# Kernel tuning notes

Hardware: AMD Instinct MI355X
Metric: run time of the kernel (lower is better)

Reference implementation:

```python
import jax, jax.numpy as jnp
import numpy as np

N_NODES = 100000
N_EDGES = 1600000
D = 64  # input_dim = hidden_dim = output_dim
EPS = 1e-12


def _sage_layer(x, src, dst, wl, bl, wr, br):
    # gather messages from source nodes: [E, D]
    msg = x[src]
    # scatter-mean onto destination nodes
    s = jax.ops.segment_sum(msg, dst, num_segments=x.shape[0])
    cnt = jax.ops.segment_sum(jnp.ones((src.shape[0], 1), x.dtype), dst, num_segments=x.shape[0])
    prop = s / jnp.maximum(cnt, 1.0)
    out = x @ wl.T + bl + prop @ wr.T + br
    # F.normalize(out, p=2, dim=1)
    norm = jnp.sqrt(jnp.sum(out * out, axis=1, keepdims=True))
    return out / jnp.maximum(norm, EPS)


def setup_inputs() -> dict:
    key = jax.random.key(0)
    ks = jax.random.split(key, 12)
    d = D

    def lin(k, fan_in, fan_out):
        bound = 1.0 / np.sqrt(fan_in)
        kw, kb = jax.random.split(k)
        w = jax.random.uniform(kw, (fan_out, fan_in), jnp.float32, -bound, bound)
        b = jax.random.uniform(kb, (fan_out,), jnp.float32, -bound, bound)
        return w, b

    x = jax.random.normal(ks[0], (N_NODES, d), jnp.float32)
    edge_index = jax.random.randint(ks[1], (2, N_EDGES), 0, N_NODES, jnp.int64)

    w1l, b1l = lin(ks[2], d, d)
    w1r, b1r = lin(ks[3], d, d)
    w2l, b2l = lin(ks[4], d, d)
    w2r, b2r = lin(ks[5], d, d)
    wp1, bp1 = lin(ks[6], d, d)
    wp2, bp2 = lin(ks[7], d, d)

    return {"x": x, "edge_index": edge_index,
            "w1l": w1l, "b1l": b1l, "w1r": w1r, "b1r": b1r,
            "w2l": w2l, "b2l": b2l, "w2r": w2r, "b2r": b2r,
            "wp1": wp1, "bp1": bp1, "wp2": wp2, "bp2": bp2}


def reference(x, edge_index, w1l, b1l, w1r, b1r, w2l, b2l, w2r, b2r, wp1, bp1, wp2, bp2):
    src = edge_index[0]
    dst = edge_index[1]
    # layer 1: GraphSage -> relu (dropout is identity in eval)
    h = _sage_layer(x, src, dst, w1l, b1l, w1r, b1r)
    h = jax.nn.relu(h)
    # layer 2
    h = _sage_layer(h, src, dst, w2l, b2l, w2r, b2r)
    h = jax.nn.relu(h)
    # post_mp: Linear -> Dropout(identity) -> Linear; emb=True so no log_softmax
    h = h @ wp1.T + bp1
    h = h @ wp2.T + bp2
    return h
```

## Files before the change

### kernel.cpp

```cpp
#include <hip/hip_runtime.h>

#define NN 100000
#define NE 1600000
#define DD 64
#define NB 196
#define BKT 512
#define CAP 9000
#define NOCT 12500
#define NH 391
#define NG1 1024

__global__ void init_kernel(int* __restrict__ gcursor) {
  int t = threadIdx.x;
  if (t < NB) gcursor[t] = t * CAP;
}

__launch_bounds__(256)
__global__ void scatter2_kernel(const int* __restrict__ src, const int* __restrict__ dst,
                                int* __restrict__ gcursor, int2* __restrict__ pairs) {
  __shared__ int lh[NB];
  __shared__ int lbase[NB];
  __shared__ int lcur[NB];
  const int NQ = NE / 4;
  int t = blockIdx.x * 256 + threadIdx.x;
  const int nt = NH * 256;
  for (int i = threadIdx.x; i < NB; i += 256) lh[i] = 0;
  __syncthreads();
  int4 dv[4], sv[4];
  bool pv[4];
  #pragma unroll
  for (int k = 0; k < 4; ++k) {
    int idx = t + k * nt;
    pv[k] = idx < NQ;
    if (pv[k]) {
      dv[k] = reinterpret_cast<const int4*>(dst)[idx];
      sv[k] = reinterpret_cast<const int4*>(src)[idx];
      atomicAdd(&lh[dv[k].x >> 9], 1);
      atomicAdd(&lh[dv[k].y >> 9], 1);
      atomicAdd(&lh[dv[k].z >> 9], 1);
      atomicAdd(&lh[dv[k].w >> 9], 1);
    }
  }
  __syncthreads();
  for (int i = threadIdx.x; i < NB; i += 256) {
    lcur[i] = 0;
    lbase[i] = lh[i] ? atomicAdd(&gcursor[i], lh[i]) : 0;
  }
  __syncthreads();
  #pragma unroll
  for (int k = 0; k < 4; ++k) {
    if (pv[k]) {
      int b;
      b = dv[k].x >> 9; pairs[lbase[b] + atomicAdd(&lcur[b], 1)] = make_int2(sv[k].x, dv[k].x);
      b = dv[k].y >> 9; pairs[lbase[b] + atomicAdd(&lcur[b], 1)] = make_int2(sv[k].y, dv[k].y);
      b = dv[k].z >> 9; pairs[lbase[b] + atomicAdd(&lcur[b], 1)] = make_int2(sv[k].z, dv[k].z);
      b = dv[k].w >> 9; pairs[lbase[b] + atomicAdd(&lcur[b], 1)] = make_int2(sv[k].w, dv[k].w);
    }
  }
}

__launch_bounds__(256)
__global__ void csr_kernel(const int2* __restrict__ pairs, const int* __restrict__ gcursor,
                           int* __restrict__ deg, int* __restrict__ off,
                           int* __restrict__ adj) {
  __shared__ int lh[BKT];
  __shared__ int wsum[4];
  int b = blockIdx.x;
  int t = threadIdx.x;
  int rs = b * CAP, re = gcursor[b];
  lh[2 * t] = 0;
  lh[2 * t + 1] = 0;
  __syncthreads();
  for (int i = rs + t; i < re; i += 256)
    atomicAdd(&lh[pairs[i].y - b * BKT], 1);
  __syncthreads();
  int lane = t & 63, w = t >> 6;
  int h0 = lh[2 * t], h1 = lh[2 * t + 1];
  int s = h0 + h1, incl = s;
  #pragma unroll
  for (int o = 1; o < 64; o <<= 1) {
    int u = __shfl_up(incl, o, 64);
    if (lane >= o) incl += u;
  }
  if (lane == 63) wsum[w] = incl;
  __syncthreads();
  int prefix = 0;
  for (int u = 0; u < w; ++u) prefix += wsum[u];
  int excl = prefix + incl - s;
  int n0 = b * BKT + 2 * t, n1 = n0 + 1;
  if (n0 < NN) { deg[n0] = h0; off[n0] = rs + excl; }
  if (n1 < NN) { deg[n1] = h1; off[n1] = rs + excl + h0; }
  lh[2 * t] = excl;
  lh[2 * t + 1] = excl + h0;
  __syncthreads();
  for (int i = rs + t; i < re; i += 256) {
    int2 e = pairs[i];
    int pos = atomicAdd(&lh[e.y - b * BKT], 1);
    adj[rs + pos] = e.x;
  }
}

__launch_bounds__(256)
__global__ void selfgemm_kernel(const float* __restrict__ x,
                                const float* __restrict__ wl,
                                const float* __restrict__ bl,
                                const float* __restrict__ br,
                                float* __restrict__ tmp,
                                const float* __restrict__ wp1, const float* __restrict__ bp1,
                                const float* __restrict__ wp2, const float* __restrict__ bp2,
                                float* __restrict__ wcT, float* __restrict__ bc) {
  __shared__ float wA[DD * DD] __attribute__((aligned(16)));
  __shared__ float sp[4][8][DD] __attribute__((aligned(16)));
  int bid = blockIdx.x;
  if (bid < NG1) {
    int tid = threadIdx.x;
    int j = tid & 63;
    int w = tid >> 6;
    for (int i = tid; i < DD * DD; i += 256) {
      int jj = i >> 6, kk = i & 63;
      wA[kk * DD + jj] = wl[i];
    }
    float bias = bl[j] + br[j];
    __syncthreads();
    const int ngrp = 3125;
    for (int grp = bid; grp < ngrp; grp += NG1) {
      int n0 = (grp * 4 + w) * 8;
      #pragma unroll
      for (int i = 0; i < 8; ++i) sp[w][i][j] = x[(size_t)(n0 + i) * DD + j];
      float acc[8];
      #pragma unroll
      for (int i = 0; i < 8; ++i) acc[i] = bias;
      #pragma unroll
      for (int q = 0; q < 16; ++q) {
        int kb = q * 4;
        float w0 = wA[(kb + 0) * DD + j];
        float w1v = wA[(kb + 1) * DD + j];
        float w2v = wA[(kb + 2) * DD + j];
        float w3v = wA[(kb + 3) * DD + j];
        #pragma unroll
        for (int i = 0; i < 8; ++i) {
          float4 sv = *(const float4*)&sp[w][i][kb];
          float a = acc[i];
          a = fmaf(sv.x, w0, a);
          a = fmaf(sv.y, w1v, a);
          a = fmaf(sv.z, w2v, a);
          a = fmaf(sv.w, w3v, a);
          acc[i] = a;
        }
      }
      #pragma unroll
      for (int i = 0; i < 8; ++i) tmp[(size_t)(n0 + i) * DD + j] = acc[i];
    }
  } else {
    int t = threadIdx.x;
    for (int idx = t; idx < DD * DD; idx += 256) {
      int jp = idx >> 6, k = idx & 63;
      float s = 0.f;
      #pragma unroll
      for (int m = 0; m < DD; ++m) s = fmaf(wp2[jp * DD + m], wp1[m * DD + k], s);
      wcT[k * DD + jp] = s;
    }
    if (t < DD) {
      float s = bp2[t];
      #pragma unroll
      for (int m = 0; m < DD; ++m) s = fmaf(wp2[t * DD + m], bp1[m], s);
      bc[t] = s;
    }
  }
}

__launch_bounds__(256)
__global__ void gather_kernel(const float* __restrict__ x,
                              const int* __restrict__ off,
                              const int* __restrict__ deg,
                              const int* __restrict__ adj,
                              float* __restrict__ prop) {
  const float4* X = reinterpret_cast<const float4*>(x);
  int wid = (blockIdx.x * 256 + threadIdx.x) >> 6;
  int nwaves = (gridDim.x * 256) >> 6;
  int lane = threadIdx.x & 63;
  int g = lane >> 4;
  int s = lane & 15;
  const int NQUAD = NN / 4;
  for (int q = wid; q < NQUAD; q += nwaves) {
    int n = q * 4 + g;
    int start = off[n];
    int d = deg[n];
    float4 a0 = {0,0,0,0}, a1 = {0,0,0,0}, a2 = {0,0,0,0}, a3 = {0,0,0,0};
    int t = 0;
    for (; t + 4 <= d; t += 4) {
      int i0 = adj[start + t + 0];
      int i1 = adj[start + t + 1];
      int i2 = adj[start + t + 2];
      int i3 = adj[start + t + 3];
      float4 v0 = X[i0 * 16 + s];
      float4 v1 = X[i1 * 16 + s];
      float4 v2 = X[i2 * 16 + s];
      float4 v3 = X[i3 * 16 + s];
      a0.x += v0.x; a0.y += v0.y; a0.z += v0.z; a0.w += v0.w;
      a1.x += v1.x; a1.y += v1.y; a1.z += v1.z; a1.w += v1.w;
      a2.x += v2.x; a2.y += v2.y; a2.z += v2.z; a2.w += v2.w;
      a3.x += v3.x; a3.y += v3.y; a3.z += v3.z; a3.w += v3.w;
    }
    if (t < d) {
      int dm = d - 1;
      int u1 = (t + 1 < d) ? t + 1 : dm;
      int u2 = (t + 2 < d) ? t + 2 : dm;
      int i0 = adj[start + t];
      int i1 = adj[start + u1];
      int i2 = adj[start + u2];
      float4 v0 = X[i0 * 16 + s];
      float4 v1 = X[i1 * 16 + s];
      float4 v2 = X[i2 * 16 + s];
      a0.x += v0.x; a0.y += v0.y; a0.z += v0.z; a0.w += v0.w;
      if (t + 1 < d) { a1.x += v1.x; a1.y += v1.y; a1.z += v1.z; a1.w += v1.w; }
      if (t + 2 < d) { a2.x += v2.x; a2.y += v2.y; a2.z += v2.z; a2.w += v2.w; }
    }
    float rc = 1.0f / fmaxf((float)d, 1.0f);
    float4 r;
    r.x = ((a0.x + a1.x) + (a2.x + a3.x)) * rc;
    r.y = ((a0.y + a1.y) + (a2.y + a3.y)) * rc;
    r.z = ((a0.z + a1.z) + (a2.z + a3.z)) * rc;
    r.w = ((a0.w + a1.w) + (a2.w + a3.w)) * rc;
    reinterpret_cast<float4*>(prop)[n * 16 + s] = r;
  }
}

__launch_bounds__(512, 4)
__global__ void gemm_light_kernel(float* __restrict__ out,
                                  const float* __restrict__ prop,
                                  const float* __restrict__ wr) {
  __shared__ float wrA[DD * DD] __attribute__((aligned(16)));
  __shared__ float pp[8][8][DD] __attribute__((aligned(16)));
  int tid = threadIdx.x;
  int j = tid & 63;
  int w = tid >> 6;

  for (int i = tid; i < DD * DD; i += 512) {
    int jj = i >> 6, kk = i & 63;
    wrA[kk * DD + jj] = wr[i];
  }
  __syncthreads();

  const int ngrp = (NOCT + 7) / 8;
  for (int grp = blockIdx.x; grp < ngrp; grp += gridDim.x) {
    int o = grp * 8 + w;
    if (o >= NOCT) continue;
    int n0 = o * 8;

    float acc[8];
    #pragma unroll
    for (int i = 0; i < 8; ++i) {
      pp[w][i][j] = prop[(size_t)(n0 + i) * DD + j];
      acc[i] = out[(size_t)(n0 + i) * DD + j];
    }

    #pragma unroll
    for (int q = 0; q < 16; ++q) {
      int kb = q * 4;
      float w0 = wrA[(kb + 0) * DD + j];
      float w1v = wrA[(kb + 1) * DD + j];
      float w2v = wrA[(kb + 2) * DD + j];
      float w3v = wrA[(kb + 3) * DD + j];
      #pragma unroll
      for (int i = 0; i < 8; ++i) {
        float4 pv = *(const float4*)&pp[w][i][kb];
        float a = acc[i];
        a = fmaf(pv.x, w0, a);
        a = fmaf(pv.y, w1v, a);
        a = fmaf(pv.z, w2v, a);
        a = fmaf(pv.w, w3v, a);
        acc[i] = a;
      }
    }

    #pragma unroll
    for (int i = 0; i < 8; ++i) {
      float a = acc[i];
      float ss = a * a;
      #pragma unroll
      for (int o2 = 32; o2 > 0; o2 >>= 1) ss += __shfl_xor(ss, o2, 64);
      float ov = a / fmaxf(sqrtf(ss), 1e-12f);
      ov = fmaxf(ov, 0.0f);
      out[(size_t)(n0 + i) * DD + j] = ov;
    }
  }
}

__launch_bounds__(512, 4)
__global__ void sage_post_kernel(const float* __restrict__ xin,
                                 const float* __restrict__ prop,
                                 const float* __restrict__ wl,
                                 const float* __restrict__ bl,
                                 const float* __restrict__ wr,
                                 const float* __restrict__ br,
                                 const float* __restrict__ wcT,
                                 const float* __restrict__ bc,
                                 float* __restrict__ out) {
  __shared__ float wlA[DD * DD] __attribute__((aligned(16)));
  __shared__ float wrA[DD * DD] __attribute__((aligned(16)));
  __shared__ float sp[8][8][DD] __attribute__((aligned(16)));
  __shared__ float pp[8][8][DD] __attribute__((aligned(16)));
  int tid = threadIdx.x;
  int j = tid & 63;
  int w = tid >> 6;

  for (int i = tid; i < DD * DD; i += 512) {
    int jj = i >> 6, kk = i & 63;
    wlA[kk * DD + jj] = wl[i];
    wrA[kk * DD + jj] = wr[i];
  }
  float bias = bl[j] + br[j];
  float bcv = bc[j];
  __syncthreads();

  const int ngrp = (NOCT + 7) / 8;
  for (int grp = blockIdx.x; grp < ngrp; grp += gridDim.x) {
    int o = grp * 8 + w;
    if (o >= NOCT) continue;
    int n0 = o * 8;

    #pragma unroll
    for (int i = 0; i < 8; ++i) {
      sp[w][i][j] = xin[(size_t)(n0 + i) * DD + j];
      pp[w][i][j] = prop[(size_t)(n0 + i) * DD + j];
    }

    float acc[8];
    #pragma unroll
    for (int i = 0; i < 8; ++i) acc[i] = bias;

    #pragma unroll
    for (int q = 0; q < 16; ++q) {
      int kb = q * 4;
      float wl0 = wlA[(kb + 0) * DD + j];
      float wl1 = wlA[(kb + 1) * DD + j];
      float wl2 = wlA[(kb + 2) * DD + j];
      float wl3 = wlA[(kb + 3) * DD + j];
      float wr0 = wrA[(kb + 0) * DD + j];
      float wr1 = wrA[(kb + 1) * DD + j];
      float wr2 = wrA[(kb + 2) * DD + j];
      float wr3 = wrA[(kb + 3) * DD + j];
      #pragma unroll
      for (int i = 0; i < 8; ++i) {
        float4 sv = *(const float4*)&sp[w][i][kb];
        float4 pv = *(const float4*)&pp[w][i][kb];
        float a = acc[i];
        a = fmaf(sv.x, wl0, a);
        a = fmaf(sv.y, wl1, a);
        a = fmaf(sv.z, wl2, a);
        a = fmaf(sv.w, wl3, a);
        a = fmaf(pv.x, wr0, a);
        a = fmaf(pv.y, wr1, a);
        a = fmaf(pv.z, wr2, a);
        a = fmaf(pv.w, wr3, a);
        acc[i] = a;
      }
    }

    #pragma unroll
    for (int i = 0; i < 8; ++i) {
      float a = acc[i];
      float ss = a * a;
      #pragma unroll
      for (int o2 = 32; o2 > 0; o2 >>= 1) ss += __shfl_xor(ss, o2, 64);
      float ov = a / fmaxf(sqrtf(ss), 1e-12f);
      ov = fmaxf(ov, 0.0f);
      sp[w][i][j] = ov;
    }

    float acc2[8];
    #pragma unroll
    for (int i = 0; i < 8; ++i) acc2[i] = bcv;
    #pragma unroll
    for (int q = 0; q < 16; ++q) {
      int kb = q * 4;
      float w0 = wcT[(kb + 0) * DD + j];
      float w1v = wcT[(kb + 1) * DD + j];
      float w2v = wcT[(kb + 2) * DD + j];
      float w3v = wcT[(kb + 3) * DD + j];
      #pragma unroll
      for (int i = 0; i < 8; ++i) {
        float4 hv = *(const float4*)&sp[w][i][kb];
        float a = acc2[i];
        a = fmaf(hv.x, w0, a);
        a = fmaf(hv.y, w1v, a);
        a = fmaf(hv.z, w2v, a);
        a = fmaf(hv.w, w3v, a);
        acc2[i] = a;
      }
    }
    #pragma unroll
    for (int i = 0; i < 8; ++i) out[(size_t)(n0 + i) * DD + j] = acc2[i];
  }
}

extern "C" void kernel_launch(void* const* d_in, const int* in_sizes, int n_in,
                              void* d_out, int out_size, void* d_ws, size_t ws_size,
                              hipStream_t stream) {
  const float* x   = (const float*)d_in[0];
  const int*   ei  = (const int*)d_in[1];
  const float* w1l = (const float*)d_in[2];
  const float* b1l = (const float*)d_in[3];
  const float* w1r = (const float*)d_in[4];
  const float* b1r = (const float*)d_in[5];
  const float* w2l = (const float*)d_in[6];
  const float* b2l = (const float*)d_in[7];
  const float* w2r = (const float*)d_in[8];
  const float* b2r = (const float*)d_in[9];
  const float* wp1 = (const float*)d_in[10];
  const float* bp1 = (const float*)d_in[11];
  const float* wp2 = (const float*)d_in[12];
  const float* bp2 = (const float*)d_in[13];
  float* out = (float*)d_out;

  const int* src = ei;
  const int* dst = ei + NE;

  int* deg     = (int*)d_ws;
  int* off     = deg + 102400;
  int* aux     = off + 102400;
  int* gcursor = aux;
  float* wcT   = (float*)(aux + 1024);
  float* bc    = wcT + 4096;
  int* adj     = (int*)(bc + 1024);
  float* prop  = (float*)(adj + NB * CAP);
  int2* pairs  = (int2*)prop;

  init_kernel<<<1, 256, 0, stream>>>(gcursor);
  scatter2_kernel<<<NH, 256, 0, stream>>>(src, dst, gcursor, pairs);
  csr_kernel<<<NB, 256, 0, stream>>>(pairs, gcursor, deg, off, adj);

  selfgemm_kernel<<<NG1 + 1, 256, 0, stream>>>(x, w1l, b1l, b1r, out,
                                               wp1, bp1, wp2, bp2, wcT, bc);

  gather_kernel<<<2048, 256, 0, stream>>>(x, off, deg, adj, prop);
  gemm_light_kernel<<<1024, 512, 0, stream>>>(out, prop, w1r);

  gather_kernel<<<2048, 256, 0, stream>>>(out, off, deg, adj, prop);
  sage_post_kernel<<<512, 512, 0, stream>>>(out, prop, w2l, b2l, w2r, b2r,
                                            wcT, bc, out);
}
```

Measured before the change: 299.9 us.

## Read activations directly from global memory and pack weights as float4 in LDS

The three dense GEMM kernels stop staging the activation rows (x, prop) into shared memory. Each thread now reads float4 chunks straight from global memory, as wave-uniform broadcast loads. Weight matrices are stored in an interleaved float4 layout so each k-quad is one 16-byte LDS read, and the combined post-MLP weight is written in the same layout. Launch bounds rise to 6 blocks per unit and sage_post gets more blocks. The aim is to cut LDS traffic and footprint to raise occupancy, at the risk of more global or L1 load instructions and register pressure.

```diff
diff --git a/kernel.cpp b/kernel.cpp
--- a/kernel.cpp
+++ b/kernel.cpp
@@ -100,7 +100,7 @@
   }
 }
 
-__launch_bounds__(256)
+__launch_bounds__(256, 6)
 __global__ void selfgemm_kernel(const float* __restrict__ x,
                                 const float* __restrict__ wl,
                                 const float* __restrict__ bl,
@@ -108,43 +108,38 @@
                                 float* __restrict__ tmp,
                                 const float* __restrict__ wp1, const float* __restrict__ bp1,
                                 const float* __restrict__ wp2, const float* __restrict__ bp2,
-                                float* __restrict__ wcT, float* __restrict__ bc) {
-  __shared__ float wA[DD * DD] __attribute__((aligned(16)));
-  __shared__ float sp[4][8][DD] __attribute__((aligned(16)));
+                                float* __restrict__ wc4, float* __restrict__ bc) {
+  __shared__ float4 wlA4[16 * 64] __attribute__((aligned(16)));
   int bid = blockIdx.x;
   if (bid < NG1) {
     int tid = threadIdx.x;
     int j = tid & 63;
     int w = tid >> 6;
+    float* wlf = (float*)wlA4;
     for (int i = tid; i < DD * DD; i += 256) {
-      int jj = i >> 6, kk = i & 63;
-      wA[kk * DD + jj] = wl[i];
+      int jj = i >> 6, k = i & 63;
+      wlf[(((k >> 2) * 64) + jj) * 4 + (k & 3)] = wl[i];
     }
     float bias = bl[j] + br[j];
     __syncthreads();
     const int ngrp = 3125;
     for (int grp = bid; grp < ngrp; grp += NG1) {
       int n0 = (grp * 4 + w) * 8;
-      #pragma unroll
-      for (int i = 0; i < 8; ++i) sp[w][i][j] = x[(size_t)(n0 + i) * DD + j];
       float acc[8];
       #pragma unroll
       for (int i = 0; i < 8; ++i) acc[i] = bias;
       #pragma unroll
       for (int q = 0; q < 16; ++q) {
         int kb = q * 4;
-        float w0 = wA[(kb + 0) * DD + j];
-        float w1v = wA[(kb + 1) * DD + j];
-        float w2v = wA[(kb + 2) * DD + j];
-        float w3v = wA[(kb + 3) * DD + j];
+        float4 wq = wlA4[q * 64 + j];
         #pragma unroll
         for (int i = 0; i < 8; ++i) {
-          float4 sv = *(const float4*)&sp[w][i][kb];
+          float4 sv = *(const float4*)&x[(size_t)(n0 + i) * DD + kb];
           float a = acc[i];
-          a = fmaf(sv.x, w0, a);
-          a = fmaf(sv.y, w1v, a);
-          a = fmaf(sv.z, w2v, a);
-          a = fmaf(sv.w, w3v, a);
+          a = fmaf(sv.x, wq.x, a);
+          a = fmaf(sv.y, wq.y, a);
+          a = fmaf(sv.z, wq.z, a);
+          a = fmaf(sv.w, wq.w, a);
           acc[i] = a;
         }
       }
@@ -158,7 +153,7 @@
       float s = 0.f;
       #pragma unroll
       for (int m = 0; m < DD; ++m) s = fmaf(wp2[jp * DD + m], wp1[m * DD + k], s);
-      wcT[k * DD + jp] = s;
+      wc4[(((k >> 2) * 64) + jp) * 4 + (k & 3)] = s;
     }
     if (t < DD) {
       float s = bp2[t];
@@ -226,19 +221,18 @@
   }
 }
 
-__launch_bounds__(512, 4)
+__launch_bounds__(512, 6)
 __global__ void gemm_light_kernel(float* __restrict__ out,
                                   const float* __restrict__ prop,
                                   const float* __restrict__ wr) {
-  __shared__ float wrA[DD * DD] __attribute__((aligned(16)));
-  __shared__ float pp[8][8][DD] __attribute__((aligned(16)));
+  __shared__ float4 wrA4[16 * 64] __attribute__((aligned(16)));
   int tid = threadIdx.x;
   int j = tid & 63;
   int w = tid >> 6;
-
+  float* wrf = (float*)wrA4;
   for (int i = tid; i < DD * DD; i += 512) {
-    int jj = i >> 6, kk = i & 63;
-    wrA[kk * DD + jj] = wr[i];
+    int jj = i >> 6, k = i & 63;
+    wrf[(((k >> 2) * 64) + jj) * 4 + (k & 3)] = wr[i];
   }
   __syncthreads();
 
@@ -250,26 +244,20 @@
 
     float acc[8];
     #pragma unroll
-    for (int i = 0; i < 8; ++i) {
-      pp[w][i][j] = prop[(size_t)(n0 + i) * DD + j];
-      acc[i] = out[(size_t)(n0 + i) * DD + j];
-    }
+    for (int i = 0; i < 8; ++i) acc[i] = out[(size_t)(n0 + i) * DD + j];
 
     #pragma unroll
     for (int q = 0; q < 16; ++q) {
       int kb = q * 4;
-      float w0 = wrA[(kb + 0) * DD + j];
-      float w1v = wrA[(kb + 1) * DD + j];
-      float w2v = wrA[(kb + 2) * DD + j];
-      float w3v = wrA[(kb + 3) * DD + j];
+      float4 wq = wrA4[q * 64 + j];
       #pragma unroll
       for (int i = 0; i < 8; ++i) {
-        float4 pv = *(const float4*)&pp[w][i][kb];
+        float4 pv = *(const float4*)&prop[(size_t)(n0 + i) * DD + kb];
         float a = acc[i];
-        a = fmaf(pv.x, w0, a);
-        a = fmaf(pv.y, w1v, a);
-        a = fmaf(pv.z, w2v, a);
-        a = fmaf(pv.w, w3v, a);
+        a = fmaf(pv.x, wq.x, a);
+        a = fmaf(pv.y, wq.y, a);
+        a = fmaf(pv.z, wq.z, a);
+        a = fmaf(pv.w, wq.w, a);
         acc[i] = a;
       }
     }
@@ -287,28 +275,29 @@
   }
 }
 
-__launch_bounds__(512, 4)
+__launch_bounds__(512, 6)
 __global__ void sage_post_kernel(const float* __restrict__ xin,
                                  const float* __restrict__ prop,
                                  const float* __restrict__ wl,
                                  const float* __restrict__ bl,
                                  const float* __restrict__ wr,
                                  const float* __restrict__ br,
-                                 const float* __restrict__ wcT,
+                                 const float4* __restrict__ wc4,
                                  const float* __restrict__ bc,
                                  float* __restrict__ out) {
-  __shared__ float wlA[DD * DD] __attribute__((aligned(16)));
-  __shared__ float wrA[DD * DD] __attribute__((aligned(16)));
+  __shared__ float4 wlA4[16 * 64] __attribute__((aligned(16)));
+  __shared__ float4 wrA4[16 * 64] __attribute__((aligned(16)));
   __shared__ float sp[8][8][DD] __attribute__((aligned(16)));
-  __shared__ float pp[8][8][DD] __attribute__((aligned(16)));
   int tid = threadIdx.x;
   int j = tid & 63;
   int w = tid >> 6;
 
+  float* wlf = (float*)wlA4;
+  float* wrf = (float*)wrA4;
   for (int i = tid; i < DD * DD; i += 512) {
-    int jj = i >> 6, kk = i & 63;
-    wlA[kk * DD + jj] = wl[i];
-    wrA[kk * DD + jj] = wr[i];
+    int jj = i >> 6, k = i & 63;
+    wlf[(((k >> 2) * 64) + jj) * 4 + (k & 3)] = wl[i];
+    wrf[(((k >> 2) * 64) + jj) * 4 + (k & 3)] = wr[i];
   }
   float bias = bl[j] + br[j];
   float bcv = bc[j];
@@ -320,12 +309,6 @@
     if (o >= NOCT) continue;
     int n0 = o * 8;
 
-    #pragma unroll
-    for (int i = 0; i < 8; ++i) {
-      sp[w][i][j] = xin[(size_t)(n0 + i) * DD + j];
-      pp[w][i][j] = prop[(size_t)(n0 + i) * DD + j];
-    }
-
     float acc[8];
     #pragma unroll
     for (int i = 0; i < 8; ++i) acc[i] = bias;
@@ -333,27 +316,21 @@
     #pragma unroll
     for (int q = 0; q < 16; ++q) {
       int kb = q * 4;
-      float wl0 = wlA[(kb + 0) * DD + j];
-      float wl1 = wlA[(kb + 1) * DD + j];
-      float wl2 = wlA[(kb + 2) * DD + j];
-      float wl3 = wlA[(kb + 3) * DD + j];
-      float wr0 = wrA[(kb + 0) * DD + j];
-      float wr1 = wrA[(kb + 1) * DD + j];
-      float wr2 = wrA[(kb + 2) * DD + j];
-      float wr3 = wrA[(kb + 3) * DD + j];
+      float4 wlq = wlA4[q * 64 + j];
+      float4 wrq = wrA4[q * 64 + j];
       #pragma unroll
       for (int i = 0; i < 8; ++i) {
-        float4 sv = *(const float4*)&sp[w][i][kb];
-        float4 pv = *(const float4*)&pp[w][i][kb];
+        float4 sv = *(const float4*)&xin[(size_t)(n0 + i) * DD + kb];
+        float4 pv = *(const float4*)&prop[(size_t)(n0 + i) * DD + kb];
         float a = acc[i];
-        a = fmaf(sv.x, wl0, a);
-        a = fmaf(sv.y, wl1, a);
-        a = fmaf(sv.z, wl2, a);
-        a = fmaf(sv.w, wl3, a);
-        a = fmaf(pv.x, wr0, a);
-        a = fmaf(pv.y, wr1, a);
-        a = fmaf(pv.z, wr2, a);
-        a = fmaf(pv.w, wr3, a);
+        a = fmaf(sv.x, wlq.x, a);
+        a = fmaf(sv.y, wlq.y, a);
+        a = fmaf(sv.z, wlq.z, a);
+        a = fmaf(sv.w, wlq.w, a);
+        a = fmaf(pv.x, wrq.x, a);
+        a = fmaf(pv.y, wrq.y, a);
+        a = fmaf(pv.z, wrq.z, a);
+        a = fmaf(pv.w, wrq.w, a);
         acc[i] = a;
       }
     }
@@ -375,18 +352,15 @@
     #pragma unroll
     for (int q = 0; q < 16; ++q) {
       int kb = q * 4;
-      float w0 = wcT[(kb + 0) * DD + j];
-      float w1v = wcT[(kb + 1) * DD + j];
-      float w2v = wcT[(kb + 2) * DD + j];
-      float w3v = wcT[(kb + 3) * DD + j];
+      float4 wq = wc4[q * 64 + j];
       #pragma unroll
       for (int i = 0; i < 8; ++i) {
         float4 hv = *(const float4*)&sp[w][i][kb];
         float a = acc2[i];
-        a = fmaf(hv.x, w0, a);
-        a = fmaf(hv.y, w1v, a);
-        a = fmaf(hv.z, w2v, a);
-        a = fmaf(hv.w, w3v, a);
+        a = fmaf(hv.x, wq.x, a);
+        a = fmaf(hv.y, wq.y, a);
+        a = fmaf(hv.z, wq.z, a);
+        a = fmaf(hv.w, wq.w, a);
         acc2[i] = a;
       }
     }
@@ -421,8 +395,8 @@
   int* off     = deg + 102400;
   int* aux     = off + 102400;
   int* gcursor = aux;
-  float* wcT   = (float*)(aux + 1024);
-  float* bc    = wcT + 4096;
+  float* wc4f  = (float*)(aux + 1024);
+  float* bc    = wc4f + 4096;
   int* adj     = (int*)(bc + 1024);
   float* prop  = (float*)(adj + NB * CAP);
   int2* pairs  = (int2*)prop;
@@ -432,12 +406,12 @@
   csr_kernel<<<NB, 256, 0, stream>>>(pairs, gcursor, deg, off, adj);
 
   selfgemm_kernel<<<NG1 + 1, 256, 0, stream>>>(x, w1l, b1l, b1r, out,
-                                               wp1, bp1, wp2, bp2, wcT, bc);
+                                               wp1, bp1, wp2, bp2, wc4f, bc);
 
   gather_kernel<<<2048, 256, 0, stream>>>(x, off, deg, adj, prop);
   gemm_light_kernel<<<1024, 512, 0, stream>>>(out, prop, w1r);
 
   gather_kernel<<<2048, 256, 0, stream>>>(out, off, deg, adj, prop);
-  sage_post_kernel<<<512, 512, 0, stream>>>(out, prop, w2l, b2l, w2r, b2r,
-                                            wcT, bc, out);
-}
+  sage_post_kernel<<<768, 512, 0, stream>>>(out, prop, w2l, b2l, w2r, b2r,
+                                            (const float4*)wc4f, bc, out);
+}
```

New measurement: 554.4 us. 84.9% more time.
